# Optimization experiments

Hardware: AMD Instinct MI355X
Metric: run time of the kernel (lower is better)

## Reference

```python
import jax, jax.numpy as jnp
import numpy as np

IN_C, OUT_C = 128, 256
KH, KW = 3, 3
STRIDE = (1, 1)
PAD = (1, 1)


def setup_inputs() -> dict:
    key = jax.random.key(0)
    kx, kw = jax.random.split(key)
    x = jax.random.normal(kx, (32, IN_C, 56, 56), dtype=jnp.float32)
    k = 1.0 / (IN_C * KH * KW)
    weight = (2.0 * jax.random.uniform(kw, (OUT_C, IN_C, KH, KW), dtype=jnp.float32) - 1.0) * (k ** 0.5)
    return {"x": x, "weight": weight}


def reference(x, weight):
    # Equivalent to the as_strided broadcast-multiply-sum: a plain 2D cross-correlation
    # (no bias), NCHW input, OIHW weight, stride (1,1), padding (1,1).
    return jax.lax.conv_general_dilated(
        x, weight,
        window_strides=STRIDE,
        padding=[(PAD[0], PAD[0]), (PAD[1], PAD[1])],
        dimension_numbers=("NCHW", "OIHW", "NCHW"),
    )
```

## Files before the change

### kernel.cpp

```cpp
#include <hip/hip_runtime.h>

typedef __attribute__((ext_vector_type(8))) short short8;
typedef __attribute__((ext_vector_type(4))) float floatx4;

#define IN_C 128
#define OUT_C 256
#define NB 32
#define HW 56
#define S_PER_N (HW * HW)
#define M_TOTAL (NB * S_PER_N)
#define PH 58
#define PW 66
#define XN_ELEMS (NB * PH * PW * IN_C)
#define WT_ELEMS (9 * OUT_C * IN_C)
#define XF_BLOCKS (PH * NB)
#define WF_BLOCKS (WT_ELEMS / 256)

__device__ __forceinline__ unsigned short f2bf(float f) {
    unsigned int u = __builtin_bit_cast(unsigned int, f);
    u = (u + 0x7FFFu + ((u >> 16) & 1u)) >> 16;
    return (unsigned short)u;
}

__device__ __forceinline__ void gld_lds16(const unsigned short* g, unsigned short* l) {
    __builtin_amdgcn_global_load_lds(
        (const __attribute__((address_space(1))) unsigned int*)g,
        (__attribute__((address_space(3))) unsigned int*)l, 16, 0, 0);
}

__global__ void xform_all(const float* __restrict__ x, const float* __restrict__ w,
                          unsigned short* __restrict__ xn, unsigned short* __restrict__ wt) {
    const int bid = blockIdx.x;
    const int tid = threadIdx.x;

    if (bid >= XF_BLOCKS) {
        const int idx = (bid - XF_BLOCKS) * 256 + tid;
        const int ic  = idx & 127;
        const int oc  = (idx >> 7) & 255;
        const int khw = idx >> 15;
        wt[idx] = f2bf(w[(oc * IN_C + ic) * 9 + khw]);
        return;
    }

    const int ihp = bid % PH;
    const int n   = bid / PH;
    unsigned int* __restrict__ row32 =
        (unsigned int*)(xn + (size_t)(n * PH + ihp) * PW * IN_C);
    const int WORDS = PW * IN_C / 2;

    if (ihp == 0 || ihp == PH - 1) {
        for (int i = tid; i < WORDS; i += 256) row32[i] = 0u;
        return;
    }
    if (tid < 128) {
        int p = (tid >> 6) * (PW - 1);
        row32[p * 64 + (tid & 63)] = 0u;
    }
    const int ih = ihp - 1;
    const float* __restrict__ xrow = x + (size_t)n * IN_C * S_PER_N + (size_t)ih * HW;
    unsigned long long* __restrict__ row64 = (unsigned long long*)row32;
#pragma unroll
    for (int t = 0; t < 2; ++t) {
        const int item = tid + t * 256;
        if (item >= 32 * 14) break;
        const int icw2 = item & 31;
        const int pix4 = item >> 5;
        const float* cbase = xrow + (size_t)(4 * icw2) * S_PER_N + pix4 * 4;
        const float4 v0 = *(const float4*)(cbase);
        const float4 v1 = *(const float4*)(cbase + S_PER_N);
        const float4 v2 = *(const float4*)(cbase + 2 * S_PER_N);
        const float4 v3 = *(const float4*)(cbase + 3 * S_PER_N);
        unsigned long long* o = row64 + (size_t)(pix4 * 4 + 1) * 32 + icw2;
#define PACK2(a, b, c, d) ((unsigned long long)((unsigned int)f2bf(a) | ((unsigned int)f2bf(b) << 16)) \
                         | ((unsigned long long)((unsigned int)f2bf(c) | ((unsigned int)f2bf(d) << 16)) << 32))
        o[0]  = PACK2(v0.x, v1.x, v2.x, v3.x);
        o[32] = PACK2(v0.y, v1.y, v2.y, v3.y);
        o[64] = PACK2(v0.z, v1.z, v2.z, v3.z);
        o[96] = PACK2(v0.w, v1.w, v2.w, v3.w);
#undef PACK2
    }
}

__global__ void __launch_bounds__(256, 4)
conv_mfma(const unsigned short* __restrict__ xn,
          const unsigned short* __restrict__ wt,
          float* __restrict__ out) {
    const int tid  = threadIdx.x;
    const int lane = tid & 63;
    const int wv   = tid >> 6;
    const int l15  = lane & 15;
    const int quad = lane >> 4;
    const int fr7  = l15 & 7;

    const int bx0 = blockIdx.x;
    const int bx  = (bx0 & 7) * 196 + (bx0 >> 3);
    const int tile_oc = bx & 1;
    const int tile_m  = bx >> 1;

    const int s_blk  = tile_m * 128;
    const int oc_blk = tile_oc * 128;

    __shared__ unsigned short A_lds[128 * 64];
    __shared__ unsigned short B_lds[128 * 64];

    const int srow = tid >> 3;
    const int sic  = ((tid & 7) ^ (srow & 7)) * 8;

    unsigned int aoff[4], boff[4];
#pragma unroll
    for (int q = 0; q < 4; ++q) {
        int row = q * 32 + srow;
        aoff[q] = (unsigned int)((oc_blk + row) * IN_C + sic);
        int sg = s_blk + row;
        int n  = sg / S_PER_N;
        int r  = sg % S_PER_N;
        int oh = r / HW, ow = r % HW;
        boff[q] = (unsigned int)(((n * PH + oh) * PW + ow) * IN_C + sic);
    }

    const int slot = (quad ^ fr7) * 8;
    const int aof0 = ((wv >> 1) * 64 + l15) * 64 + slot;
    const int bof0 = ((wv & 1)  * 64 + l15) * 64 + slot;

    floatx4 acc[4][4];
#pragma unroll
    for (int i = 0; i < 4; ++i)
#pragma unroll
        for (int j = 0; j < 4; ++j) acc[i][j] = (floatx4){0.f, 0.f, 0.f, 0.f};

#pragma unroll
    for (int khw = 0; khw < 9; ++khw) {
        const int xo = ((khw / 3) * PW + (khw % 3)) * IN_C;
        const int wo = khw * OUT_C * IN_C;
#pragma unroll
        for (int h = 0; h < 2; ++h) {
            const int ic0 = h * 64;
            __syncthreads();
#pragma unroll
            for (int q = 0; q < 4; ++q) {
                gld_lds16(wt + (aoff[q] + (unsigned)(wo + ic0)), A_lds + q * 2048 + tid * 8);
                gld_lds16(xn + (boff[q] + (unsigned)(xo + ic0)), B_lds + q * 2048 + tid * 8);
            }
            __syncthreads();

#pragma unroll
            for (int kk = 0; kk < 2; ++kk) {
                const int ka = aof0 ^ (kk * 32);
                const int kb = bof0 ^ (kk * 32);
                short8 a[4], b[4];
#pragma unroll
                for (int i = 0; i < 4; ++i) a[i] = *(const short8*)(A_lds + ka + i * 1024);
#pragma unroll
                for (int j = 0; j < 4; ++j) b[j] = *(const short8*)(B_lds + kb + j * 1024);
#pragma unroll
                for (int i = 0; i < 4; ++i)
#pragma unroll
                    for (int j = 0; j < 4; ++j)
                        acc[i][j] = __builtin_amdgcn_mfma_f32_16x16x32_bf16(
                            a[i], b[j], acc[i][j], 0, 0, 0);
            }
        }
    }

    const int s0  = s_blk + (wv & 1) * 64;
    const int oc0 = oc_blk + (wv >> 1) * 64;
#pragma unroll
    for (int j = 0; j < 4; ++j) {
        int s_glob = s0 + j * 16 + l15;
        int n = s_glob / S_PER_N;
        int s = s_glob % S_PER_N;
        unsigned int obase = (unsigned int)(n * OUT_C * S_PER_N + s);
#pragma unroll
        for (int i = 0; i < 4; ++i) {
            unsigned int ooff = obase + (unsigned int)((oc0 + i * 16 + quad * 4) * S_PER_N);
#pragma unroll
            for (int r = 0; r < 4; ++r)
                out[ooff + (unsigned int)(r * S_PER_N)] = acc[i][j][r];
        }
    }
}

extern "C" void kernel_launch(void* const* d_in, const int* in_sizes, int n_in,
                              void* d_out, int out_size, void* d_ws, size_t ws_size,
                              hipStream_t stream) {
    const float* x = (const float*)d_in[0];
    const float* w = (const float*)d_in[1];
    float* out = (float*)d_out;

    unsigned short* xn = (unsigned short*)d_ws;
    unsigned short* wt = xn + XN_ELEMS;

    xform_all<<<XF_BLOCKS + WF_BLOCKS, 256, 0, stream>>>(x, w, xn, wt);
    conv_mfma<<<(M_TOTAL / 128) * 2, 256, 0, stream>>>(xn, wt, out);
}
```

Before: 201.2 us.

## Double-buffer LDS tiles with K=32 steps to overlap loads with MFMA

Restructures the conv main loop from 18 single-buffered K=64 stages into 36 double-buffered K=32 stages. Each step issues the global-to-LDS loads for the next step before running the MFMAs on the current buffer, with one waitcnt and barrier per step. The LDS layout is repacked with two rows per 64-element line and a new XOR swizzle, so total LDS stays the same. The intent is to hide global load latency behind compute. The cost is twice as many barriers, and there is a risk of LDS read races, since the code relies on the end-of-step barrier before a buffer is overwritten.

Result: slower. 208.6 us (+3.7%).

```diff
diff --git a/kernel.cpp b/kernel.cpp
--- a/kernel.cpp
+++ b/kernel.cpp
@@ -90,7 +90,6 @@
     const int wv   = tid >> 6;
     const int l15  = lane & 15;
     const int quad = lane >> 4;
-    const int fr7  = l15 & 7;
 
     const int bx0 = blockIdx.x;
     const int bx  = (bx0 & 7) * 196 + (bx0 >> 3);
@@ -100,27 +99,28 @@
     const int s_blk  = tile_m * 128;
     const int oc_blk = tile_oc * 128;
 
-    __shared__ unsigned short A_lds[128 * 64];
-    __shared__ unsigned short B_lds[128 * 64];
+    __shared__ unsigned short A_lds[2][64 * 64];
+    __shared__ unsigned short B_lds[2][64 * 64];
 
-    const int srow = tid >> 3;
-    const int sic  = ((tid & 7) ^ (srow & 7)) * 8;
+    const int s8p   = (tid & 7) ^ ((tid >> 3) & 7);
+    const int rbase = ((tid >> 3) << 1) + (s8p >> 2);
+    const int icl   = (s8p & 3) * 8;
 
-    unsigned int aoff[4], boff[4];
+    unsigned int aoff[2], boff[2];
 #pragma unroll
-    for (int q = 0; q < 4; ++q) {
-        int row = q * 32 + srow;
-        aoff[q] = (unsigned int)((oc_blk + row) * IN_C + sic);
-        int sg = s_blk + row;
+    for (int q = 0; q < 2; ++q) {
+        int r = q * 64 + rbase;
+        aoff[q] = (unsigned int)((oc_blk + r) * IN_C + icl);
+        int sg = s_blk + r;
         int n  = sg / S_PER_N;
-        int r  = sg % S_PER_N;
-        int oh = r / HW, ow = r % HW;
-        boff[q] = (unsigned int)(((n * PH + oh) * PW + ow) * IN_C + sic);
+        int rem = sg % S_PER_N;
+        int oh = rem / HW, ow = rem % HW;
+        boff[q] = (unsigned int)(((n * PH + oh) * PW + ow) * IN_C + icl);
     }
 
-    const int slot = (quad ^ fr7) * 8;
-    const int aof0 = ((wv >> 1) * 64 + l15) * 64 + slot;
-    const int bof0 = ((wv & 1)  * 64 + l15) * 64 + slot;
+    const int swz  = ((((l15 & 1) << 2) + quad) ^ (l15 >> 1)) * 8;
+    const int aof0 = (wv >> 1) * 2048 + (l15 >> 1) * 64 + swz;
+    const int bof0 = (wv & 1)  * 2048 + (l15 >> 1) * 64 + swz;
 
     floatx4 acc[4][4];
 #pragma unroll
@@ -129,37 +129,41 @@
         for (int j = 0; j < 4; ++j) acc[i][j] = (floatx4){0.f, 0.f, 0.f, 0.f};
 
 #pragma unroll
-    for (int khw = 0; khw < 9; ++khw) {
-        const int xo = ((khw / 3) * PW + (khw % 3)) * IN_C;
-        const int wo = khw * OUT_C * IN_C;
-#pragma unroll
-        for (int h = 0; h < 2; ++h) {
-            const int ic0 = h * 64;
-            __syncthreads();
-#pragma unroll
-            for (int q = 0; q < 4; ++q) {
-                gld_lds16(wt + (aoff[q] + (unsigned)(wo + ic0)), A_lds + q * 2048 + tid * 8);
-                gld_lds16(xn + (boff[q] + (unsigned)(xo + ic0)), B_lds + q * 2048 + tid * 8);
-            }
-            __syncthreads();
+    for (int q = 0; q < 2; ++q) {
+        gld_lds16(wt + aoff[q], &A_lds[0][q * 2048 + tid * 8]);
+        gld_lds16(xn + boff[q], &B_lds[0][q * 2048 + tid * 8]);
+    }
+    asm volatile("s_waitcnt vmcnt(0)" ::: "memory");
+    __builtin_amdgcn_s_barrier();
 
 #pragma unroll
-            for (int kk = 0; kk < 2; ++kk) {
-                const int ka = aof0 ^ (kk * 32);
-                const int kb = bof0 ^ (kk * 32);
-                short8 a[4], b[4];
+    for (int t = 0; t < 36; ++t) {
+        const int c = t & 1;
+        if (t < 35) {
+            const int tn   = t + 1;
+            const int khwn = tn >> 2;
+            const int subn = tn & 3;
+            const unsigned awo = (unsigned)(khwn * OUT_C * IN_C + subn * 32);
+            const unsigned bxo = (unsigned)(((khwn / 3) * PW + (khwn % 3)) * IN_C + subn * 32);
 #pragma unroll
-                for (int i = 0; i < 4; ++i) a[i] = *(const short8*)(A_lds + ka + i * 1024);
-#pragma unroll
-                for (int j = 0; j < 4; ++j) b[j] = *(const short8*)(B_lds + kb + j * 1024);
-#pragma unroll
-                for (int i = 0; i < 4; ++i)
-#pragma unroll
-                    for (int j = 0; j < 4; ++j)
-                        acc[i][j] = __builtin_amdgcn_mfma_f32_16x16x32_bf16(
-                            a[i], b[j], acc[i][j], 0, 0, 0);
+            for (int q = 0; q < 2; ++q) {
+                gld_lds16(wt + (aoff[q] + awo), &A_lds[1 - c][q * 2048 + tid * 8]);
+                gld_lds16(xn + (boff[q] + bxo), &B_lds[1 - c][q * 2048 + tid * 8]);
             }
         }
+        short8 a[4], b[4];
+#pragma unroll
+        for (int i = 0; i < 4; ++i) a[i] = *(const short8*)(&A_lds[c][0] + aof0 + i * 512);
+#pragma unroll
+        for (int j = 0; j < 4; ++j) b[j] = *(const short8*)(&B_lds[c][0] + bof0 + j * 512);
+#pragma unroll
+        for (int i = 0; i < 4; ++i)
+#pragma unroll
+            for (int j = 0; j < 4; ++j)
+                acc[i][j] = __builtin_amdgcn_mfma_f32_16x16x32_bf16(
+                    a[i], b[j], acc[i][j], 0, 0, 0);
+        asm volatile("s_waitcnt vmcnt(0)" ::: "memory");
+        __builtin_amdgcn_s_barrier();
     }
 
     const int s0  = s_blk + (wv & 1) * 64;
```
